# Performance work log

Hardware: AMD Instinct MI355X
Metric: run time of the kernel (lower is better)

## Reference

```python
import jax, jax.numpy as jnp
import numpy as np

OLD_CL = 16
RATIO = 1.0
IGNORE_INDEX = 255


def setup_inputs() -> dict:
    key = jax.random.key(0)
    k1, k2 = jax.random.split(key)
    N, C, H, W = 8, 21, 512, 512
    inputs = jax.random.normal(k1, (N, C, H, W), dtype=jnp.float32)
    targets = jax.random.randint(k2, (N, H, W), 0, C).astype(jnp.int32)
    return {"inputs": inputs, "targets": targets}


def _forward(inputs, targets):
    N, C, H, W = inputs.shape
    # unbiased log-prob remap: old classes collapsed into channel 0
    den = jax.nn.logsumexp(inputs, axis=1)                       # [N,H,W]
    out0 = jax.nn.logsumexp(inputs[:, :OLD_CL], axis=1) - den    # [N,H,W]
    outputs = jnp.zeros_like(inputs)                             # channels 1..OLD_CL-1 stay 0
    outputs = outputs.at[:, 0].set(out0)
    outputs = outputs.at[:, OLD_CL:].set(inputs[:, OLD_CL:] - den[:, None])

    labels = jnp.where(targets < OLD_CL, 0, targets)             # [N,H,W]

    # per-sample class histogram (device-side replacement for the per-sample
    # cpu torch.histc loop). histc(bins=C, min=0, max=C-1) on integer-valued
    # labels counts occurrences per class, dropping values outside [0, C-1].
    lab_flat = labels.reshape(N, -1)
    in_range = lab_flat < C
    seg = jnp.where(in_range, lab_flat, 0) + jnp.arange(N, dtype=lab_flat.dtype)[:, None] * C
    hist = jax.ops.segment_sum(
        in_range.astype(jnp.float32).reshape(-1), seg.reshape(-1), num_segments=N * C
    ).reshape(N, C)

    cls = jnp.arange(C)
    idx_old = (cls < OLD_CL) & (cls != 0)                        # [C], old classes except 0
    idx0 = hist == 0                                             # computed on raw hist
    hist = hist.at[:, 0].set(hist[:, :OLD_CL].sum(axis=1))
    hist = jnp.where(idx_old[None, :], 0.0, hist)
    hist = jnp.where(idx0 & ~idx_old[None, :], 1.0, hist)
    weight = jnp.power(hist.sum(axis=1, keepdims=True) / hist, RATIO)
    weight = jnp.where(idx_old[None, :], 0.0, weight)            # kills the infs from /0
    weight = jax.lax.stop_gradient(weight)                       # torch .detach()

    outputs = outputs * weight[:, :, None, None]

    # nll_loss with ignore_index, mean reduction over valid pixels
    valid = labels != IGNORE_INDEX
    safe = jnp.where(valid, labels, 0)
    picked = jnp.take_along_axis(outputs, safe[:, None], axis=1)[:, 0]  # [N,H,W]
    vmask = valid.astype(outputs.dtype)
    return -(picked * vmask).sum() / vmask.sum()


def reference(inputs, targets):
    return _forward(inputs, targets)
```

## Files before the change

### kernel.cpp

```cpp
#include <hip/hip_runtime.h>

#define NS 8
#define NC 21
#define HW (512*512)
#define OLD 16
#define IGNORE_IDX 255
#define HBLK 64
#define LBLK 64
#define LITER 4

#define HPART_OFF 0
#define WGT_OFF   16384
#define SUM_OFF   17408
#define CNT_OFF   17416

__device__ __forceinline__ float get4(const float4& v, int j) {
    switch (j) { case 0: return v.x; case 1: return v.y; case 2: return v.z; default: return v.w; }
}

__global__ void __launch_bounds__(256) hist_kernel(const int* __restrict__ tgt,
                                                   int* __restrict__ hpart) {
    int n   = blockIdx.x >> 6;
    int blk = blockIdx.x & 63;
    const int4* t4 = reinterpret_cast<const int4*>(tgt + (size_t)n * HW);
    int c[6] = {0, 0, 0, 0, 0, 0};
#pragma unroll
    for (int it = 0; it < 4; ++it) {
        int idx = blk * 1024 + it * 256 + threadIdx.x;
        int4 t = t4[idx];
#define COUNT_LAB(T) { int lab = (T) < OLD ? 0 : (T);                       \
        c[0] += (lab == 0);  c[1] += (lab == 16); c[2] += (lab == 17);      \
        c[3] += (lab == 18); c[4] += (lab == 19); c[5] += (lab == 20); }
        COUNT_LAB(t.x) COUNT_LAB(t.y) COUNT_LAB(t.z) COUNT_LAB(t.w)
#undef COUNT_LAB
    }
#pragma unroll
    for (int off = 32; off > 0; off >>= 1)
#pragma unroll
        for (int k = 0; k < 6; ++k) c[k] += __shfl_down(c[k], off, 64);

    __shared__ int sh[4][6];
    int wave = threadIdx.x >> 6;
    if ((threadIdx.x & 63) == 0)
#pragma unroll
        for (int k = 0; k < 6; ++k) sh[wave][k] = c[k];
    __syncthreads();
    if (threadIdx.x == 0) {
        int* o = hpart + blockIdx.x * 8;
#pragma unroll
        for (int k = 0; k < 6; ++k)
            o[k] = sh[0][k] + sh[1][k] + sh[2][k] + sh[3][k];
    }
}

__global__ void weight_kernel(const int* __restrict__ hpart,
                              float* __restrict__ wgt,
                              double* __restrict__ sum_acc,
                              int* __restrict__ cnt_acc) {
    __shared__ int shist[NS][6];
    int t = threadIdx.x;
    if (t < NS * 6) {
        int n = t / 6, k = t % 6;
        int s = 0;
        for (int b = 0; b < HBLK; ++b) s += hpart[(n * HBLK + b) * 8 + k];
        shist[n][k] = s;
    }
    if (t == 0) { *sum_acc = 0.0; *cnt_acc = 0; }
    __syncthreads();
    if (t < NS * NC) {
        int n = t / NC, c = t % NC;
        float h[6];
        float total = 0.0f;
#pragma unroll
        for (int k = 0; k < 6; ++k) {
            int raw = shist[n][k];
            h[k] = (raw == 0) ? 1.0f : (float)raw;
            total += h[k];
        }
        float w;
        if (c >= 1 && c < OLD)      w = 0.0f;
        else if (c == 0)            w = total / h[0];
        else                        w = total / h[c - OLD + 1];
        wgt[t] = w;
    }
}

__global__ void __launch_bounds__(256) loss_kernel(const float* __restrict__ in,
                                                   const int* __restrict__ tgt,
                                                   const float* __restrict__ wgt,
                                                   double* __restrict__ sum_acc,
                                                   int* __restrict__ cnt_acc) {
    int n   = blockIdx.x / LBLK;
    int blk = blockIdx.x % LBLK;

    __shared__ float sw[NC];
    if (threadIdx.x < NC) sw[threadIdx.x] = wgt[n * NC + threadIdx.x];
    __syncthreads();

    const float* inN = in + (size_t)n * (NC * HW);
    const int4*  t4  = reinterpret_cast<const int4*>(tgt + (size_t)n * HW);

    float partial = 0.0f;
    int cnt = 0;

#pragma unroll 1
    for (int it = 0; it < LITER; ++it) {
        int g = (blk * LITER + it) * 256 + threadIdx.x;
        int p = g * 4;
        int4 t = t4[g];

        float4 v[NC];
#pragma unroll
        for (int c = 0; c < NC; ++c)
            v[c] = *reinterpret_cast<const float4*>(inN + (size_t)c * HW + p);

        int labs[4] = {t.x, t.y, t.z, t.w};
#pragma unroll
        for (int j = 0; j < 4; ++j) {
            int lab = labs[j];
            lab = lab < OLD ? 0 : lab;
            float m16 = -3.4e38f;
#pragma unroll
            for (int c = 0; c < OLD; ++c) m16 = fmaxf(m16, get4(v[c], j));
            float s16 = 0.0f;
#pragma unroll
            for (int c = 0; c < OLD; ++c) s16 += __expf(get4(v[c], j) - m16);
            float m = m16;
#pragma unroll
            for (int c = OLD; c < NC; ++c) m = fmaxf(m, get4(v[c], j));
            float s  = s16 * __expf(m16 - m);
            float xl = 0.0f;
#pragma unroll
            for (int c = OLD; c < NC; ++c) {
                float x = get4(v[c], j);
                s += __expf(x - m);
                xl = (lab == c) ? x : xl;
            }
            float den   = m + __logf(s);
            float lse16 = m16 + __logf(s16);
            float val   = (lab == 0 ? lse16 : xl) - den;
            int  widx   = (lab < NC) ? lab : 0;
            bool valid  = (lab != IGNORE_IDX);
            if (valid) { partial += sw[widx] * val; cnt++; }
        }
    }

#pragma unroll
    for (int off = 32; off > 0; off >>= 1) {
        partial += __shfl_down(partial, off, 64);
        cnt     += __shfl_down(cnt, off, 64);
    }
    __shared__ float sp[4];
    __shared__ int   sc[4];
    int wave = threadIdx.x >> 6;
    if ((threadIdx.x & 63) == 0) { sp[wave] = partial; sc[wave] = cnt; }
    __syncthreads();
    if (threadIdx.x == 0) {
        atomicAdd(sum_acc, (double)(sp[0] + sp[1] + sp[2] + sp[3]));
        atomicAdd(cnt_acc, sc[0] + sc[1] + sc[2] + sc[3]);
    }
}

__global__ void finalize_kernel(const double* __restrict__ sum_acc,
                                const int* __restrict__ cnt_acc,
                                float* __restrict__ out) {
    if (threadIdx.x == 0) {
        int c = *cnt_acc;
        out[0] = (c > 0) ? (float)(-(*sum_acc) / (double)c) : 0.0f;
    }
}

extern "C" void kernel_launch(void* const* d_in, const int* in_sizes, int n_in,
                              void* d_out, int out_size, void* d_ws, size_t ws_size,
                              hipStream_t stream) {
    const float* inputs  = (const float*)d_in[0];
    const int*   targets = (const int*)d_in[1];
    float*       out     = (float*)d_out;

    char* ws = (char*)d_ws;
    int*    hpart   = (int*)(ws + HPART_OFF);
    float*  wgt     = (float*)(ws + WGT_OFF);
    double* sum_acc = (double*)(ws + SUM_OFF);
    int*    cnt_acc = (int*)(ws + CNT_OFF);

    hist_kernel<<<NS * HBLK, 256, 0, stream>>>(targets, hpart);
    weight_kernel<<<1, 256, 0, stream>>>(hpart, wgt, sum_acc, cnt_acc);
    loss_kernel<<<NS * LBLK, 256, 0, stream>>>(inputs, targets, wgt, sum_acc, cnt_acc);
    finalize_kernel<<<1, 64, 0, stream>>>(sum_acc, cnt_acc, out);
}
```

Before: 256.4 us.

## Fuse histogram into loss pass and apply class weights in finalize

Computes per-class sums of log-prob values and per-class counts in a single pass over inputs and targets, then applies the class-frequency weights algebraically in a single finalize kernel. This removes the separate histogram and weight kernels, one read of the targets, and the global atomics. The finalize kernel does more serial work, and ignore-index handling is now implicit through the class matching.

```diff
diff --git a/kernel.cpp b/kernel.cpp
--- a/kernel.cpp
+++ b/kernel.cpp
@@ -4,104 +4,25 @@
 #define NC 21
 #define HW (512*512)
 #define OLD 16
-#define IGNORE_IDX 255
-#define HBLK 64
 #define LBLK 64
 #define LITER 4
+#define PSTRIDE 16
 
-#define HPART_OFF 0
-#define WGT_OFF   16384
-#define SUM_OFF   17408
-#define CNT_OFF   17416
 
 __device__ __forceinline__ float get4(const float4& v, int j) {
     switch (j) { case 0: return v.x; case 1: return v.y; case 2: return v.z; default: return v.w; }
 }
 
-__global__ void __launch_bounds__(256) hist_kernel(const int* __restrict__ tgt,
-                                                   int* __restrict__ hpart) {
+__global__ void __launch_bounds__(256) loss_hist_kernel(const float* __restrict__ in,
+                                                        const int* __restrict__ tgt,
+                                                        float* __restrict__ part) {
     int n   = blockIdx.x >> 6;
     int blk = blockIdx.x & 63;
-    const int4* t4 = reinterpret_cast<const int4*>(tgt + (size_t)n * HW);
-    int c[6] = {0, 0, 0, 0, 0, 0};
-#pragma unroll
-    for (int it = 0; it < 4; ++it) {
-        int idx = blk * 1024 + it * 256 + threadIdx.x;
-        int4 t = t4[idx];
-#define COUNT_LAB(T) { int lab = (T) < OLD ? 0 : (T);                       \
-        c[0] += (lab == 0);  c[1] += (lab == 16); c[2] += (lab == 17);      \
-        c[3] += (lab == 18); c[4] += (lab == 19); c[5] += (lab == 20); }
-        COUNT_LAB(t.x) COUNT_LAB(t.y) COUNT_LAB(t.z) COUNT_LAB(t.w)
-#undef COUNT_LAB
-    }
-#pragma unroll
-    for (int off = 32; off > 0; off >>= 1)
-#pragma unroll
-        for (int k = 0; k < 6; ++k) c[k] += __shfl_down(c[k], off, 64);
-
-    __shared__ int sh[4][6];
-    int wave = threadIdx.x >> 6;
-    if ((threadIdx.x & 63) == 0)
-#pragma unroll
-        for (int k = 0; k < 6; ++k) sh[wave][k] = c[k];
-    __syncthreads();
-    if (threadIdx.x == 0) {
-        int* o = hpart + blockIdx.x * 8;
-#pragma unroll
-        for (int k = 0; k < 6; ++k)
-            o[k] = sh[0][k] + sh[1][k] + sh[2][k] + sh[3][k];
-    }
-}
-
-__global__ void weight_kernel(const int* __restrict__ hpart,
-                              float* __restrict__ wgt,
-                              double* __restrict__ sum_acc,
-                              int* __restrict__ cnt_acc) {
-    __shared__ int shist[NS][6];
-    int t = threadIdx.x;
-    if (t < NS * 6) {
-        int n = t / 6, k = t % 6;
-        int s = 0;
-        for (int b = 0; b < HBLK; ++b) s += hpart[(n * HBLK + b) * 8 + k];
-        shist[n][k] = s;
-    }
-    if (t == 0) { *sum_acc = 0.0; *cnt_acc = 0; }
-    __syncthreads();
-    if (t < NS * NC) {
-        int n = t / NC, c = t % NC;
-        float h[6];
-        float total = 0.0f;
-#pragma unroll
-        for (int k = 0; k < 6; ++k) {
-            int raw = shist[n][k];
-            h[k] = (raw == 0) ? 1.0f : (float)raw;
-            total += h[k];
-        }
-        float w;
-        if (c >= 1 && c < OLD)      w = 0.0f;
-        else if (c == 0)            w = total / h[0];
-        else                        w = total / h[c - OLD + 1];
-        wgt[t] = w;
-    }
-}
-
-__global__ void __launch_bounds__(256) loss_kernel(const float* __restrict__ in,
-                                                   const int* __restrict__ tgt,
-                                                   const float* __restrict__ wgt,
-                                                   double* __restrict__ sum_acc,
-                                                   int* __restrict__ cnt_acc) {
-    int n   = blockIdx.x / LBLK;
-    int blk = blockIdx.x % LBLK;
-
-    __shared__ float sw[NC];
-    if (threadIdx.x < NC) sw[threadIdx.x] = wgt[n * NC + threadIdx.x];
-    __syncthreads();
-
     const float* inN = in + (size_t)n * (NC * HW);
     const int4*  t4  = reinterpret_cast<const int4*>(tgt + (size_t)n * HW);
 
-    float partial = 0.0f;
-    int cnt = 0;
+    float s[6]  = {0.f, 0.f, 0.f, 0.f, 0.f, 0.f};
+    int   cnt[6] = {0, 0, 0, 0, 0, 0};
 
 #pragma unroll 1
     for (int it = 0; it < LITER; ++it) {
@@ -128,45 +49,102 @@
             float m = m16;
 #pragma unroll
             for (int c = OLD; c < NC; ++c) m = fmaxf(m, get4(v[c], j));
-            float s  = s16 * __expf(m16 - m);
+            float sm = s16 * __expf(m16 - m);
             float xl = 0.0f;
 #pragma unroll
             for (int c = OLD; c < NC; ++c) {
                 float x = get4(v[c], j);
-                s += __expf(x - m);
+                sm += __expf(x - m);
                 xl = (lab == c) ? x : xl;
             }
-            float den   = m + __logf(s);
+            float den   = m + __logf(sm);
             float lse16 = m16 + __logf(s16);
             float val   = (lab == 0 ? lse16 : xl) - den;
-            int  widx   = (lab < NC) ? lab : 0;
-            bool valid  = (lab != IGNORE_IDX);
-            if (valid) { partial += sw[widx] * val; cnt++; }
+
+            bool h0 = (lab == 0);
+            s[0]  += h0 ? val : 0.0f;  cnt[0] += h0;
+#pragma unroll
+            for (int k = 1; k < 6; ++k) {
+                bool hk = (lab == 15 + k);
+                s[k]  += hk ? val : 0.0f;
+                cnt[k] += hk;
+            }
         }
     }
 
 #pragma unroll
-    for (int off = 32; off > 0; off >>= 1) {
-        partial += __shfl_down(partial, off, 64);
-        cnt     += __shfl_down(cnt, off, 64);
-    }
-    __shared__ float sp[4];
-    __shared__ int   sc[4];
+    for (int off = 32; off > 0; off >>= 1)
+#pragma unroll
+        for (int k = 0; k < 6; ++k) {
+            s[k]   += __shfl_down(s[k], off, 64);
+            cnt[k] += __shfl_down(cnt[k], off, 64);
+        }
+
+    __shared__ float sp[4][6];
+    __shared__ int   sc[4][6];
     int wave = threadIdx.x >> 6;
-    if ((threadIdx.x & 63) == 0) { sp[wave] = partial; sc[wave] = cnt; }
+    if ((threadIdx.x & 63) == 0)
+#pragma unroll
+        for (int k = 0; k < 6; ++k) { sp[wave][k] = s[k]; sc[wave][k] = cnt[k]; }
     __syncthreads();
-    if (threadIdx.x == 0) {
-        atomicAdd(sum_acc, (double)(sp[0] + sp[1] + sp[2] + sp[3]));
-        atomicAdd(cnt_acc, sc[0] + sc[1] + sc[2] + sc[3]);
+    if (threadIdx.x < 6) {
+        int k = threadIdx.x;
+        float fs = sp[0][k] + sp[1][k] + sp[2][k] + sp[3][k];
+        int   ic = sc[0][k] + sc[1][k] + sc[2][k] + sc[3][k];
+        part[(size_t)blockIdx.x * PSTRIDE + k] = fs;
+        ((int*)part)[(size_t)blockIdx.x * PSTRIDE + 8 + k] = ic;
     }
 }
 
-__global__ void finalize_kernel(const double* __restrict__ sum_acc,
-                                const int* __restrict__ cnt_acc,
-                                float* __restrict__ out) {
-    if (threadIdx.x == 0) {
-        int c = *cnt_acc;
-        out[0] = (c > 0) ? (float)(-(*sum_acc) / (double)c) : 0.0f;
+__global__ void finalize_kernel(const float* __restrict__ part, float* __restrict__ out) {
+    __shared__ double    ssum[NS][6];
+    __shared__ int       shist[NS][6];
+    __shared__ double    wsum[NS];
+    __shared__ long long wcnt[NS];
+    int t = threadIdx.x;
+
+    if (t < NS * 12) {
+        int n = t / 12, v = t % 12;
+        if (v < 6) {
+            double a = 0.0;
+            for (int b = 0; b < LBLK; ++b)
+                a += (double)part[(size_t)(n * LBLK + b) * PSTRIDE + v];
+            ssum[n][v] = a;
+        } else {
+            int k = v - 6, a = 0;
+            const int* ip = (const int*)part;
+            for (int b = 0; b < LBLK; ++b)
+                a += ip[(size_t)(n * LBLK + b) * PSTRIDE + 8 + k];
+            shist[n][k] = a;
+        }
+    }
+    __syncthreads();
+
+    if (t < NS) {
+        float h[6];
+        float total = 0.0f;
+        long long c = 0;
+#pragma unroll
+        for (int k = 0; k < 6; ++k) {
+            int raw = shist[t][k];
+            h[k] = (raw == 0) ? 1.0f : (float)raw;
+            total += h[k];
+            c += raw;
+        }
+        double acc = 0.0;
+#pragma unroll
+        for (int k = 0; k < 6; ++k)
+            acc += (double)(total / h[k]) * ssum[t][k];
+        wsum[t] = acc;
+        wcnt[t] = c;
+    }
+    __syncthreads();
+
+    if (t == 0) {
+        double S = 0.0;
+        long long C = 0;
+        for (int n = 0; n < NS; ++n) { S += wsum[n]; C += wcnt[n]; }
+        out[0] = (C > 0) ? (float)(-S / (double)C) : 0.0f;
     }
 }
 
@@ -176,15 +154,8 @@
     const float* inputs  = (const float*)d_in[0];
     const int*   targets = (const int*)d_in[1];
     float*       out     = (float*)d_out;
+    float*       part    = (float*)d_ws;
 
-    char* ws = (char*)d_ws;
-    int*    hpart   = (int*)(ws + HPART_OFF);
-    float*  wgt     = (float*)(ws + WGT_OFF);
-    double* sum_acc = (double*)(ws + SUM_OFF);
-    int*    cnt_acc = (int*)(ws + CNT_OFF);
-
-    hist_kernel<<<NS * HBLK, 256, 0, stream>>>(targets, hpart);
-    weight_kernel<<<1, 256, 0, stream>>>(hpart, wgt, sum_acc, cnt_acc);
-    loss_kernel<<<NS * LBLK, 256, 0, stream>>>(inputs, targets, wgt, sum_acc, cnt_acc);
-    finalize_kernel<<<1, 64, 0, stream>>>(sum_acc, cnt_acc, out);
+    loss_hist_kernel<<<NS * LBLK, 256, 0, stream>>>(inputs, targets, part);
+    finalize_kernel<<<1, 128, 0, stream>>>(part, out);
 }
```

New measurement: 259.7 us. About the same (+1.3%).
